# Performance work log

Hardware: AMD Instinct MI355X
Metric: run time of the kernel (lower is better)

Reference implementation:

```python
import jax, jax.numpy as jnp
import numpy as np

NF = 16            # num_frequencies
S = 2              # scale_factor
MAX_STD = 0.5
POS_LIMIT = 1.0


def setup_inputs() -> dict:
    key = jax.random.key(0)
    ks = jax.random.split(key, 8)
    B, G, H, W = 16, 256, 128, 128
    hidden, base = 1024, 256
    in_dim = (G + 2 * NF + 1) * S * S  # 4624
    # xavier-uniform-like scales
    lim1 = float(np.sqrt(6.0 / (hidden + in_dim)))
    lim2 = float(np.sqrt(6.0 / (base + hidden)))
    return {
        "position": jax.random.uniform(ks[0], (B, 4), dtype=jnp.float32),
        "gestalt": jax.random.normal(ks[1], (B, G), dtype=jnp.float32),
        "mask": jax.random.uniform(ks[2], (B, 1, H, W), dtype=jnp.float32),
        "depth": jax.random.normal(ks[3], (B, 1, H, W), dtype=jnp.float32),
        "weight1": jax.random.uniform(ks[4], (hidden, in_dim), minval=-lim1, maxval=lim1, dtype=jnp.float32),
        "bias1": jnp.zeros((hidden,), dtype=jnp.float32),
        "weight2": jax.random.uniform(ks[5], (base, hidden), minval=-lim2, maxval=lim2, dtype=jnp.float32),
        "bias2": jnp.zeros((base,), dtype=jnp.float32),
    }


def reference(position, gestalt, mask, depth, weight1, bias1, weight2, bias2):
    B, _, H, W = mask.shape
    # positional grids in [-1, 1], shapes (1,1,H,W)
    gx = (jnp.arange(W, dtype=jnp.float32) / (W - 1)) * 2 - 1
    gy = (jnp.arange(H, dtype=jnp.float32) / (H - 1)) * 2 - 1
    grid_y, grid_x = jnp.meshgrid(gy, gx, indexing="ij")
    grid_x = grid_x[None, None]
    grid_y = grid_y[None, None]

    x = jnp.clip(position[:, 0], -POS_LIMIT, POS_LIMIT)[:, None, None, None]
    y = jnp.clip(position[:, 1], -POS_LIMIT, POS_LIMIT)[:, None, None, None]
    min_std = 1.0 / min(H, W)
    std = 0.1 / jnp.clip(position[:, 3], min_std, MAX_STD)[:, None, None, None]
    std_y = std
    std_x = std * (W / H)

    half_pi = jnp.float32(np.pi / 2)
    ngx = (grid_x - x) * std_x * half_pi  # (B,1,H,W)
    ngy = (grid_y - y) * std_y * half_pi
    freqs = (2.0 ** jnp.arange(NF, dtype=jnp.float32))[None, :, None, None]
    cos_x = jnp.cos(ngx * freqs)  # (B,NF,H,W)
    cos_y = jnp.cos(ngy * freqs)
    # interleave: [cx0, cy0, cx1, cy1, ...]
    embedding = jnp.stack([cos_x, cos_y], axis=2).reshape(B, 2 * NF, H, W)

    inp = jnp.concatenate(
        [gestalt[:, :, None, None] * mask, embedding * mask, depth * mask], axis=1
    )  # (B,C,H,W)
    C = inp.shape[1]
    # space-to-depth patchify
    p = inp.reshape(B, C, H // S, S, W // S, S)
    p = p.transpose(0, 2, 4, 1, 3, 5).reshape(B * (H // S) * (W // S), C * S * S)

    h = p @ weight1.T + bias1
    h = h * jax.nn.sigmoid(h)  # SiLU
    o = h @ weight2.T + bias2
    return o.reshape(B, H // S, W // S, -1).transpose(0, 3, 1, 2)
```

## Files before the change

kernel.cpp:

```cpp
#include <hip/hip_runtime.h>
#include <cstdio>


#define NFREQ 16
#define BB 16
#define G 256
#define KIN 1156
#define K1 144
#define STAGE_U16 12800
#define NSTAGE 6

typedef unsigned short u16;
using bf16x8 = __bf16 __attribute__((ext_vector_type(8)));
using f32x16 = float __attribute__((ext_vector_type(16)));
using f32x4  = float __attribute__((ext_vector_type(4)));

__device__ __forceinline__ u16 f2bf(float f) {
  unsigned u = __float_as_uint(f);
  u += 0x7fffu + ((u >> 16) & 1u);
  return (u16)(u >> 16);
}
__device__ __forceinline__ unsigned pk2(float a, float b) {
  return (unsigned)f2bf(a) | ((unsigned)f2bf(b) << 16);
}
__device__ __forceinline__ unsigned pk2f(float a, float b) {
  unsigned ua = __float_as_uint(a) + 0x8000u;
  unsigned ub = __float_as_uint(b) + 0x8000u;
  return __builtin_amdgcn_perm(ub, ua, 0x07060302u);
}
__device__ __forceinline__ float silu(float h) {
  float e = __builtin_amdgcn_exp2f(h * -1.44269504088896f);
  return h * __builtin_amdgcn_rcpf(1.f + e);
}
__device__ __forceinline__ void gl_lds16(const u16* g, u16* l) {
  __builtin_amdgcn_global_load_lds(
      (const __attribute__((address_space(1))) void*)g,
      (__attribute__((address_space(3))) void*)l, 16, 0, 0);
}

__global__ void k_pre(const float* __restrict__ pos,
                      const float* __restrict__ gestalt,
                      const float* __restrict__ w1,
                      const float* __restrict__ w2,
                      const float* __restrict__ bias1,
                      float* __restrict__ cosx, float* __restrict__ cosy,
                      u16* __restrict__ B1FS, u16* __restrict__ B1FB,
                      u16* __restrict__ W2F) {
  const int bid = blockIdx.x;
  const int t = threadIdx.x;

  if (bid < 1024) {
    __shared__ float w1row[KIN];
    __shared__ float gestT[G * 17];
    __shared__ float psum[256];
    __shared__ float wg[64];
    const int n = bid;
    const float b1v = bias1[n];
#pragma unroll
    for (int i = t; i < KIN; i += 256) w1row[i] = w1[(size_t)n * KIN + i];
#pragma unroll
    for (int i = t; i < BB * G; i += 256) {
      int bb = i >> 8, c = i & 255;
      gestT[c * 17 + bb] = gestalt[i];
    }
    __syncthreads();
    {
      int bb = t & 15, j = (t >> 4) & 3, q = t >> 6;
      float acc = 0.f;
#pragma unroll 8
      for (int c = q * 64; c < q * 64 + 64; ++c)
        acc += gestT[c * 17 + bb] * w1row[4 * c + j];
      psum[t] = acc;
    }
    __syncthreads();
    if (t < 64) {
      int bb = t >> 2, j = t & 3;
      wg[t] = psum[j * 16 + bb] + psum[64 + j * 16 + bb] +
              psum[128 + j * 16 + bb] + psum[192 + j * 16 + bb];
    }
    __syncthreads();
    const int ch = n >> 5, l31n = n & 31;
    if (t < 48) {
      int bb, kc;
      if (t < 16) { bb = 0; kc = t; }
      else        { bb = (t - 16) >> 1; kc = 16 + ((t - 16) & 1); }
      int k0 = kc * 8;
      float v[8];
#pragma unroll
      for (int i = 0; i < 8; ++i) {
        int k = k0 + i;
        float vv;
        if (k < 64)       vv = w1row[1024 + 8 * (k >> 2) + (k & 3)];
        else if (k < 128) { int kk = k - 64; vv = w1row[1024 + 8 * (kk >> 2) + 4 + (kk & 3)]; }
        else if (k < 132) vv = wg[bb * 4 + (k - 128)];
        else if (k < 136) vv = w1row[1152 + (k - 132)];
        else if (k == 136) vv = b1v;
        else              vv = 0.f;
        v[i] = vv;
      }
      uint4 u;
      u.x = pk2(v[0], v[1]); u.y = pk2(v[2], v[3]);
      u.z = pk2(v[4], v[5]); u.w = pk2(v[6], v[7]);
      if (kc < 16) {
        size_t idx0 = (((size_t)ch * 8 + (kc >> 1)) * 64 + (kc & 1) * 32 + l31n) * 8;
        *(uint4*)(B1FS + idx0) = u;
      } else {
        size_t idx0 = (((size_t)bb * 32 + ch) * 64 + (kc - 16) * 32 + l31n) * 8;
        *(uint4*)(B1FB + idx0) = u;
      }
    }
  } else if (bid < 1152) {
    int e8 = (bid - 1024) * 256 + t;
    int lane = e8 & 63;
    int ct   = (e8 >> 6) & 7;
    int kc   = e8 >> 9;
    int n2 = ct * 32 + (lane & 31);
    int k2 = kc * 16 + (lane >> 5) * 8;
    const float* src = w2 + (size_t)n2 * 1024 + k2;
    uint4 u;
    u.x = pk2(src[0], src[1]); u.y = pk2(src[2], src[3]);
    u.z = pk2(src[4], src[5]); u.w = pk2(src[6], src[7]);
    *(uint4*)(W2F + (size_t)e8 * 8) = u;
  } else {
    int idx = (bid - 1152) * 256 + t;
    int table = idx >> 15;
    int rem = idx & 32767;
    int b = rem >> 11;
    int f = (rem >> 7) & 15;
    int c = rem & 127;
    float p0 = pos[b * 4 + 0];
    float p1 = pos[b * 4 + 1];
    float p3 = pos[b * 4 + 3];
    float x = fminf(fmaxf(p0, -1.f), 1.f);
    float y = fminf(fmaxf(p1, -1.f), 1.f);
    float stdv = 0.1f / fminf(fmaxf(p3, 0.0078125f), 0.5f);
    const float half_pi = 1.57079632679489661923f;
    float g = ((float)c / 127.0f) * 2.0f - 1.0f;
    float ng = (table == 0) ? ((g - x) * stdv) * half_pi
                            : ((g - y) * stdv) * half_pi;
    float freq = (float)(1 << f);
    float val = cosf(ng * freq);
    if (table == 0) cosx[(b * NFREQ + f) * 128 + c] = val;
    else            cosy[(b * NFREQ + f) * 128 + c] = val;
  }
}


__device__ __forceinline__ f32x16 mfma_bf16(bf16x8 a, bf16x8 b, f32x16 c) {
  return __builtin_amdgcn_mfma_f32_32x32x16_bf16(a, b, c, 0, 0, 0);
}

__device__ __forceinline__ void gemm1(const u16* afb, const bf16x8* bfr, int lane8,
                                      const f32x16& ZERO, f32x16& a1a, f32x16& a1b) {
  bf16x8 af0 = *(const bf16x8*)(afb + 0 * 512 + lane8);
  bf16x8 af1 = *(const bf16x8*)(afb + 1 * 512 + lane8);
  a1a = mfma_bf16(af0, bfr[0], ZERO);
  a1b = mfma_bf16(af1, bfr[1], ZERO);
#pragma unroll
  for (int ks = 1; ks < 4; ++ks) {
    bf16x8 afa = *(const bf16x8*)(afb + (2 * ks) * 512 + lane8);
    bf16x8 afc = *(const bf16x8*)(afb + (2 * ks + 1) * 512 + lane8);
    a1a = mfma_bf16(afa, bfr[2 * ks], a1a);
    a1b = mfma_bf16(afc, bfr[2 * ks + 1], a1b);
  }
  bf16x8 af8 = *(const bf16x8*)(afb + 8 * 512 + lane8);
  a1a = mfma_bf16(af8, bfr[8], a1a);
}

__device__ __forceinline__ void gemm2(const u16* wfb, int lane8,
                                      bf16x8 fA, bf16x8 fB, f32x16* acc2) {
#pragma unroll
  for (int ct = 0; ct < 8; ++ct) {
    bf16x8 wf = *(const bf16x8*)(wfb + ct * 512 + lane8);
    acc2[ct] = mfma_bf16(fA, wf, acc2[ct]);
  }
#pragma unroll
  for (int ct = 0; ct < 8; ++ct) {
    bf16x8 wf = *(const bf16x8*)(wfb + 4096 + ct * 512 + lane8);
    acc2[ct] = mfma_bf16(fB, wf, acc2[ct]);
  }
}

__device__ __forceinline__ void silupack(const f32x16& a1a, const f32x16& a1b,
                                         bf16x8& fragA, bf16x8& fragB) {
  unsigned d[8];
#pragma unroll
  for (int q = 0; q < 4; ++q) {
    float s0 = silu(a1a[4 * q + 0] + a1b[4 * q + 0]);
    float s1 = silu(a1a[4 * q + 1] + a1b[4 * q + 1]);
    float s2 = silu(a1a[4 * q + 2] + a1b[4 * q + 2]);
    float s3 = silu(a1a[4 * q + 3] + a1b[4 * q + 3]);
    d[2 * q]     = pk2f(s0, s1);
    d[2 * q + 1] = pk2f(s2, s3);
  }
  unsigned e0 = d[0], e1 = d[2];
  unsigned e2 = d[1], e3 = d[3];
  unsigned e4 = d[4], e5 = d[6];
  unsigned e6 = d[5], e7 = d[7];
  asm("v_permlane32_swap_b32 %0, %1" : "+v"(e0), "+v"(e1));
  asm("v_permlane32_swap_b32 %0, %1" : "+v"(e2), "+v"(e3));
  asm("v_permlane32_swap_b32 %0, %1" : "+v"(e4), "+v"(e5));
  asm("v_permlane32_swap_b32 %0, %1" : "+v"(e6), "+v"(e7));
  uint4 fav, fbv;
  fav.x = e0; fav.y = e2; fav.z = e1; fav.w = e3;
  fbv.x = e4; fbv.y = e6; fbv.z = e5; fbv.w = e7;
  fragA = __builtin_bit_cast(bf16x8, fav);
  fragB = __builtin_bit_cast(bf16x8, fbv);
}

__global__ __launch_bounds__(512, 2) void k_main(
    const u16* __restrict__ B1FS, const u16* __restrict__ B1FB,
    const u16* __restrict__ W2F,
    const float* __restrict__ mask, const float* __restrict__ depth,
    const float* __restrict__ cosx, const float* __restrict__ cosy,
    const float* __restrict__ bias2, float* __restrict__ out)
{
  __shared__ __align__(16) u16 sbuf[NSTAGE * STAGE_U16];
  float* stg = (float*)sbuf;

  const int tid = threadIdx.x;
  const int w = tid >> 6;
  const int lane = tid & 63;
  const int lane8 = lane * 8;
  const int l31 = lane & 31;
  const int lhi = lane >> 5;
  const bool gA = (w < 4);
  const int bswz = (blockIdx.x & 7) * 32 + (blockIdx.x >> 3);
  const int r0 = bswz * 256;
  const int b = r0 >> 12;
  const int oy0 = (r0 >> 6) & 63;

  {
    const float4* cx4 = (const float4*)(cosx + (size_t)b * 2048);
    ((float4*)stg)[tid] = cx4[tid];
    if (tid < 128)
      stg[2048 + tid] = cosy[((size_t)b * 16 + (tid >> 3)) * 128 + 2 * oy0 + (tid & 7)];
    if (tid < 256) {
      ((float4*)(stg + 2176))[tid] = ((const float4*)(mask  + ((size_t)b * 128 + 2 * oy0) * 128))[tid];
      ((float4*)(stg + 3200))[tid] = ((const float4*)(depth + ((size_t)b * 128 + 2 * oy0) * 128))[tid];
    }
  }
  __syncthreads();

  bf16x8 bfr[9];
  {
    const int r = w * 32 + l31;
    const int oyl = r >> 6, ox = r & 63;
    float m[4], dd[4];
#pragma unroll
    for (int j = 0; j < 4; ++j) {
      int sy = j >> 1, sx = j & 1;
      float mv = stg[2176 + (2 * oyl + sy) * 128 + 2 * ox + sx];
      m[j] = mv;
      dd[j] = stg[3200 + (2 * oyl + sy) * 128 + 2 * ox + sx] * mv;
    }
#pragma unroll
    for (int ks = 0; ks < 9; ++ks) {
      const int k0 = ks * 16 + lhi * 8;
      unsigned dwords[4];
#pragma unroll
      for (int h = 0; h < 4; ++h) {
        float v[2];
#pragma unroll
        for (int p = 0; p < 2; ++p) {
          const int k = k0 + 2 * h + p;
          float vv;
          if (k < 64) {
            const int f = k >> 2, j = k & 3;
            vv = m[j] * stg[f * 128 + 2 * ox + (j & 1)];
          } else if (k < 128) {
            const int kk = k - 64, f = kk >> 2, j = kk & 3;
            vv = m[j] * stg[2048 + f * 8 + 2 * oyl + (j >> 1)];
          } else if (k < 132) {
            vv = m[k - 128];
          } else if (k < 136) {
            vv = dd[k - 132];
          } else if (k == 136) {
            vv = 1.0f;
          } else {
            vv = 0.f;
          }
          v[p] = vv;
        }
        dwords[h] = pk2(v[0], v[1]);
      }
      uint4 u; u.x = dwords[0]; u.y = dwords[1]; u.z = dwords[2]; u.w = dwords[3];
      bfr[ks] = __builtin_bit_cast(bf16x8, u);
    }
  }
  __syncthreads();

  f32x16 acc2[8];
#pragma unroll
  for (int c = 0; c < 8; ++c)
#pragma unroll
    for (int i = 0; i < 16; ++i) acc2[c][i] = 0.f;

  f32x16 ZERO;
#pragma unroll
  for (int i = 0; i < 16; ++i) ZERO[i] = 0.f;

  const u16* apre_s = B1FS + lane8;
  const u16* apre_b = B1FB + (size_t)b * 16384 + lane8;
  const u16* wpre   = W2F + lane8;

  auto prefetchP = [&](u16* dst) {
    gl_lds16(apre_s + w * 512, dst + w * 512);
    if (w == 7) gl_lds16(apre_b, dst + 8 * 512);
    gl_lds16(wpre + w * 512, dst + (9 + w) * 512);
    gl_lds16(wpre + (8 + w) * 512, dst + (17 + w) * 512);
    apre_s += 4096; apre_b += 512; wpre += 8192;
  };

  prefetchP(sbuf);
  prefetchP(sbuf + STAGE_U16);
  prefetchP(sbuf + 2 * STAGE_U16);

  bf16x8 fragA, fragB;
  f32x16 pa, pb;

  {
    if (w == 7) asm volatile("s_waitcnt vmcnt(4)" ::: "memory");
    else        asm volatile("s_waitcnt vmcnt(3)" ::: "memory");
    __builtin_amdgcn_s_barrier();
    asm volatile("" ::: "memory");
    __builtin_amdgcn_sched_barrier(0);
    prefetchP(sbuf + 3 * STAGE_U16);

    f32x16 a1a, a1b;
    __builtin_amdgcn_s_setprio(1);
    gemm1(sbuf, bfr, lane8, ZERO, a1a, a1b);
    __builtin_amdgcn_s_setprio(0);
    if (gA) {
      silupack(a1a, a1b, fragA, fragB);
    } else {
      pa = a1a; pb = a1b;
    }
  }

  int st = 1;
  int stw = 4;
  for (int ch = 1; ch < 32; ++ch) {
    if (!(ch & 1)) {
      if (ch == 30) asm volatile("s_waitcnt vmcnt(0)" ::: "memory");
      else if (w == 7) asm volatile("s_waitcnt vmcnt(4)" ::: "memory");
      else             asm volatile("s_waitcnt vmcnt(3)" ::: "memory");
      __builtin_amdgcn_s_barrier();
      asm volatile("" ::: "memory");
      __builtin_amdgcn_sched_barrier(0);
    }
    if (ch + 3 < 32) prefetchP(sbuf + stw * STAGE_U16);
    stw = (stw + 1 == NSTAGE) ? 0 : stw + 1;

    const u16* afb  = sbuf + st * STAGE_U16;
    const int  stp  = (st == 0) ? NSTAGE - 1 : st - 1;
    const u16* wfbp = sbuf + stp * STAGE_U16 + 4608;

    if (gA) {
      f32x16 a1a, a1b;
      __builtin_amdgcn_s_setprio(1);
      gemm1(afb, bfr, lane8, ZERO, a1a, a1b);
      gemm2(wfbp, lane8, fragA, fragB, acc2);
      __builtin_amdgcn_s_setprio(0);
      silupack(a1a, a1b, fragA, fragB);
    } else {
      silupack(pa, pb, fragA, fragB);
      f32x16 a1a, a1b;
      __builtin_amdgcn_s_setprio(1);
      gemm1(afb, bfr, lane8, ZERO, a1a, a1b);
      gemm2(wfbp, lane8, fragA, fragB, acc2);
      __builtin_amdgcn_s_setprio(0);
      pa = a1a; pb = a1b;
    }
    st = (st + 1 == NSTAGE) ? 0 : st + 1;
  }

  if (!gA) silupack(pa, pb, fragA, fragB);
  gemm2(sbuf + 1 * STAGE_U16 + 4608, lane8, fragA, fragB, acc2);

#pragma unroll
  for (int ct = 0; ct < 8; ++ct) {
    const int n2 = ct * 32 + l31;
    const float b2 = bias2[n2];
    float* ob = out + ((size_t)b * 256 + n2) * 4096;
#pragma unroll
    for (int q = 0; q < 4; ++q) {
      const int rl = w * 32 + 8 * q + 4 * lhi;
      const int oy = oy0 + (rl >> 6);
      const int ox = rl & 63;
      f32x4 v;
      v[0] = acc2[ct][4 * q + 0] + b2;
      v[1] = acc2[ct][4 * q + 1] + b2;
      v[2] = acc2[ct][4 * q + 2] + b2;
      v[3] = acc2[ct][4 * q + 3] + b2;
      *(f32x4*)(ob + oy * 64 + ox) = v;
    }
  }
}


extern "C" void kernel_launch(void* const* d_in, const int* in_sizes, int n_in,
                              void* d_out, int out_size, void* d_ws, size_t ws_size,
                              hipStream_t stream) {
  const float* pos     = (const float*)d_in[0];
  const float* gestalt = (const float*)d_in[1];
  const float* mask    = (const float*)d_in[2];
  const float* depth   = (const float*)d_in[3];
  const float* w1      = (const float*)d_in[4];
  const float* bias1   = (const float*)d_in[5];
  const float* w2      = (const float*)d_in[6];
  const float* bias2   = (const float*)d_in[7];
  float* out = (float*)d_out;

  const size_t NEED = 131072u + 131072u + 262144u + 524288u + 524288u;
  if (ws_size < NEED) {
    fprintf(stderr, "[kernel] ws_size=%zu < needed %zu — skipping launches\n",
            ws_size, NEED);
    return;
  }
  char* ws = (char*)d_ws;
  float* cosx = (float*)(ws);
  float* cosy = (float*)(ws + 131072);
  u16*   B1FS = (u16*)(ws + 262144);
  u16*   B1FB = (u16*)(ws + 262144 + 262144);
  u16*   W2F  = (u16*)(ws + 262144 + 262144 + 524288);

  k_pre<<<1408, 256, 0, stream>>>(pos, gestalt, w1, w2, bias1, cosx, cosy,
                                  B1FS, B1FB, W2F);
  k_main<<<256, 512, 0, stream>>>(B1FS, B1FB, W2F, mask, depth, cosx, cosy,
                                  bias2, out);
}
```

Before: 149.9 us.

## Load half of weight1 fragments directly to registers, shrink LDS stages

Measured after the change: 153.7 us. 2.6% more time.

```diff
diff --git a/kernel.cpp b/kernel.cpp
--- a/kernel.cpp
+++ b/kernel.cpp
@@ -7,7 +7,7 @@
 #define G 256
 #define KIN 1156
 #define K1 144
-#define STAGE_U16 12800
+#define STAGE_U16 10752
 #define NSTAGE 6
 
 typedef unsigned short u16;
@@ -150,20 +150,22 @@
   return __builtin_amdgcn_mfma_f32_32x32x16_bf16(a, b, c, 0, 0, 0);
 }
 
-__device__ __forceinline__ void gemm1(const u16* afb, const bf16x8* bfr, int lane8,
-                                      const f32x16& ZERO, f32x16& a1a, f32x16& a1b) {
-  bf16x8 af0 = *(const bf16x8*)(afb + 0 * 512 + lane8);
-  bf16x8 af1 = *(const bf16x8*)(afb + 1 * 512 + lane8);
-  a1a = mfma_bf16(af0, bfr[0], ZERO);
-  a1b = mfma_bf16(af1, bfr[1], ZERO);
-#pragma unroll
-  for (int ks = 1; ks < 4; ++ks) {
-    bf16x8 afa = *(const bf16x8*)(afb + (2 * ks) * 512 + lane8);
-    bf16x8 afc = *(const bf16x8*)(afb + (2 * ks + 1) * 512 + lane8);
-    a1a = mfma_bf16(afa, bfr[2 * ks], a1a);
-    a1b = mfma_bf16(afc, bfr[2 * ks + 1], a1b);
-  }
-  bf16x8 af8 = *(const bf16x8*)(afb + 8 * 512 + lane8);
+__device__ __forceinline__ void gemm1r(const bf16x8* afr, const u16* afl,
+                                       const bf16x8* bfr, int lane8,
+                                       const f32x16& ZERO, f32x16& a1a, f32x16& a1b) {
+  a1a = mfma_bf16(afr[0], bfr[0], ZERO);
+  a1b = mfma_bf16(afr[1], bfr[1], ZERO);
+  a1a = mfma_bf16(afr[2], bfr[2], a1a);
+  a1b = mfma_bf16(afr[3], bfr[3], a1b);
+  bf16x8 af4 = *(const bf16x8*)(afl + 0 * 512 + lane8);
+  bf16x8 af5 = *(const bf16x8*)(afl + 1 * 512 + lane8);
+  a1a = mfma_bf16(af4, bfr[4], a1a);
+  a1b = mfma_bf16(af5, bfr[5], a1b);
+  bf16x8 af6 = *(const bf16x8*)(afl + 2 * 512 + lane8);
+  bf16x8 af7 = *(const bf16x8*)(afl + 3 * 512 + lane8);
+  a1a = mfma_bf16(af6, bfr[6], a1a);
+  a1b = mfma_bf16(af7, bfr[7], a1b);
+  bf16x8 af8 = *(const bf16x8*)(afl + 4 * 512 + lane8);
   a1a = mfma_bf16(af8, bfr[8], a1a);
 }
 
@@ -224,7 +226,6 @@
   const int lane8 = lane * 8;
   const int l31 = lane & 31;
   const int lhi = lane >> 5;
-  const bool gA = (w < 4);
   const int bswz = (blockIdx.x & 7) * 32 + (blockIdx.x >> 3);
   const int r0 = bswz * 256;
   const int b = r0 >> 12;
@@ -305,78 +306,78 @@
   const u16* wpre   = W2F + lane8;
 
   auto prefetchP = [&](u16* dst) {
-    gl_lds16(apre_s + w * 512, dst + w * 512);
-    if (w == 7) gl_lds16(apre_b, dst + 8 * 512);
-    gl_lds16(wpre + w * 512, dst + (9 + w) * 512);
-    gl_lds16(wpre + (8 + w) * 512, dst + (17 + w) * 512);
+    if (w < 4)       gl_lds16(apre_s + (4 + w) * 512, dst + w * 512);
+    else if (w == 4) gl_lds16(apre_b,                 dst + 4 * 512);
+    gl_lds16(wpre + w * 512,       dst + 2560 + w * 512);
+    gl_lds16(wpre + (8 + w) * 512, dst + 2560 + (8 + w) * 512);
     apre_s += 4096; apre_b += 512; wpre += 8192;
+  };
+
+  const u16* aglob = B1FS + lane8;
+  bf16x8 afrA[4], afrB[4];
+  auto loadAF = [&](bf16x8* afr) {
+    afr[0] = *(const bf16x8*)(aglob + 0 * 512);
+    afr[1] = *(const bf16x8*)(aglob + 1 * 512);
+    afr[2] = *(const bf16x8*)(aglob + 2 * 512);
+    afr[3] = *(const bf16x8*)(aglob + 3 * 512);
+    aglob += 4096;
+  };
+
+  bf16x8 fragA, fragB;
+
+  auto computeStep = [&](const bf16x8* afr, int stC, int stP, bool doG2) {
+    const u16* afl = sbuf + stC * STAGE_U16;
+    const u16* wfp = sbuf + stP * STAGE_U16 + 2560;
+    f32x16 a1a, a1b;
+    __builtin_amdgcn_s_setprio(1);
+    gemm1r(afr, afl, bfr, lane8, ZERO, a1a, a1b);
+    if (doG2) gemm2(wfp, lane8, fragA, fragB, acc2);
+    __builtin_amdgcn_s_setprio(0);
+    silupack(a1a, a1b, fragA, fragB);
   };
 
   prefetchP(sbuf);
   prefetchP(sbuf + STAGE_U16);
   prefetchP(sbuf + 2 * STAGE_U16);
-
-  bf16x8 fragA, fragB;
-  f32x16 pa, pb;
-
-  {
-    if (w == 7) asm volatile("s_waitcnt vmcnt(4)" ::: "memory");
-    else        asm volatile("s_waitcnt vmcnt(3)" ::: "memory");
-    __builtin_amdgcn_s_barrier();
-    asm volatile("" ::: "memory");
-    __builtin_amdgcn_sched_barrier(0);
-    prefetchP(sbuf + 3 * STAGE_U16);
-
-    f32x16 a1a, a1b;
-    __builtin_amdgcn_s_setprio(1);
-    gemm1(sbuf, bfr, lane8, ZERO, a1a, a1b);
-    __builtin_amdgcn_s_setprio(0);
-    if (gA) {
-      silupack(a1a, a1b, fragA, fragB);
-    } else {
-      pa = a1a; pb = a1b;
-    }
-  }
+  loadAF(afrA);
+  __syncthreads();
+
+  loadAF(afrB);
+  prefetchP(sbuf + 3 * STAGE_U16);
+  computeStep(afrA, 0,  5, false);
 
   int st = 1;
   int stw = 4;
-  for (int ch = 1; ch < 32; ++ch) {
-    if (!(ch & 1)) {
-      if (ch == 30) asm volatile("s_waitcnt vmcnt(0)" ::: "memory");
-      else if (w == 7) asm volatile("s_waitcnt vmcnt(4)" ::: "memory");
-      else             asm volatile("s_waitcnt vmcnt(3)" ::: "memory");
+#pragma unroll 1
+  for (int k = 0; k < 15; ++k) {
+    {
+      const int ch = 2 * k + 1;
+      loadAF(afrA);
+      if (ch + 3 <= 31) prefetchP(sbuf + stw * STAGE_U16);
+      stw = (stw + 1 == NSTAGE) ? 0 : stw + 1;
+      const int stP = (st == 0) ? NSTAGE - 1 : st - 1;
+      computeStep(afrB, st, stP, true);
+      st = (st + 1 == NSTAGE) ? 0 : st + 1;
+    }
+    {
+      const int ch = 2 * k + 2;
+      if (ch == 30)    asm volatile("s_waitcnt vmcnt(0)" ::: "memory");
+      else if (w <= 4) asm volatile("s_waitcnt vmcnt(3)" ::: "memory");
+      else             asm volatile("s_waitcnt vmcnt(2)" ::: "memory");
       __builtin_amdgcn_s_barrier();
       asm volatile("" ::: "memory");
       __builtin_amdgcn_sched_barrier(0);
-    }
-    if (ch + 3 < 32) prefetchP(sbuf + stw * STAGE_U16);
-    stw = (stw + 1 == NSTAGE) ? 0 : stw + 1;
-
-    const u16* afb  = sbuf + st * STAGE_U16;
-    const int  stp  = (st == 0) ? NSTAGE - 1 : st - 1;
-    const u16* wfbp = sbuf + stp * STAGE_U16 + 4608;
-
-    if (gA) {
-      f32x16 a1a, a1b;
-      __builtin_amdgcn_s_setprio(1);
-      gemm1(afb, bfr, lane8, ZERO, a1a, a1b);
-      gemm2(wfbp, lane8, fragA, fragB, acc2);
-      __builtin_amdgcn_s_setprio(0);
-      silupack(a1a, a1b, fragA, fragB);
-    } else {
-      silupack(pa, pb, fragA, fragB);
-      f32x16 a1a, a1b;
-      __builtin_amdgcn_s_setprio(1);
-      gemm1(afb, bfr, lane8, ZERO, a1a, a1b);
-      gemm2(wfbp, lane8, fragA, fragB, acc2);
-      __builtin_amdgcn_s_setprio(0);
-      pa = a1a; pb = a1b;
-    }
-    st = (st + 1 == NSTAGE) ? 0 : st + 1;
-  }
-
-  if (!gA) silupack(pa, pb, fragA, fragB);
-  gemm2(sbuf + 1 * STAGE_U16 + 4608, lane8, fragA, fragB, acc2);
+      loadAF(afrB);
+      if (ch + 3 <= 31) prefetchP(sbuf + stw * STAGE_U16);
+      stw = (stw + 1 == NSTAGE) ? 0 : stw + 1;
+      const int stP = (st == 0) ? NSTAGE - 1 : st - 1;
+      computeStep(afrA, st, stP, true);
+      st = (st + 1 == NSTAGE) ? 0 : st + 1;
+    }
+  }
+
+  computeStep(afrB, 1, 0, true);
+  gemm2(sbuf + 1 * STAGE_U16 + 2560, lane8, fragA, fragB, acc2);
 
 #pragma unroll
   for (int ct = 0; ct < 8; ++ct) {
```
